# Optimization experiments

Hardware: AMD Instinct MI355X
Metric: run time of the kernel (lower is better)

## Reference

```python
import jax, jax.numpy as jnp
import numpy as np

B, H = 8, 8
C_IN, C_OUT = 128, 128
E, O = C_IN // H, C_OUT // H              # per-head channels
S = (32, 32, 64)                           # spatial dims (space_dims_q == space_dims_kv)
M = (8, 8, 8)                              # lowest-mode block kept per rfft dim
N_MODES = M[0] * M[1] * M[2]               # 512 = mask.sum()
SCALE = 1.0 / (C_IN * C_OUT)


def setup_inputs() -> dict:
    key = jax.random.key(0)
    k1, k2, k3, k4 = jax.random.split(key, 4)
    q = jax.random.normal(k1, (B, H, E) + S, dtype=jnp.float32)
    k = jax.random.normal(k2, (B, H, E) + S, dtype=jnp.float32)
    # torch.rand(..., dtype=cfloat): real and imag parts each uniform [0,1), scaled
    w_re = jax.random.uniform(k3, (H, E, O, N_MODES), dtype=jnp.float32) * SCALE
    w_im = jax.random.uniform(k4, (H, E, O, N_MODES), dtype=jnp.float32) * SCALE
    return {"q": q, "k": k, "w_re": w_re, "w_im": w_im}


def _select_modes(x_ft):
    # block low-mode mask -> slice + flatten (C order, matches torch bool indexing)
    m0, m1, m2 = M
    return x_ft[..., :m0, :m1, :m2].reshape(x_ft.shape[:3] + (-1,))


def reference(q, k, w_re, w_im):
    m0, m1, m2 = M
    xq_ft = jnp.fft.rfftn(q, axes=(3, 4, 5), norm='ortho')   # [B,H,E,32,32,33] c64
    xk_ft = jnp.fft.rfftn(k, axes=(3, 4, 5), norm='ortho')
    xq_sel = _select_modes(xq_ft)                             # [B,H,E,Mq]
    xk_sel = _select_modes(xk_ft)                             # [B,H,E,Mkv]
    w = jax.lax.complex(w_re, w_im)                           # [H,E,O,Mq]

    # complex attention: no conjugation, complex tanh (matches torch)
    att = jnp.tanh(jnp.einsum('bhex,bhey->bhxy', xq_sel, xk_sel))
    xqkv = jnp.einsum('bhxy,bhey->bhex', att, xk_sel)         # [B,H,E,Mq]
    xqkvw = jnp.einsum('bhex,heox->bhox', xqkv, w)            # [B,H,O,Mq]

    out_ft = jnp.zeros((q.shape[0], H, O, S[0], S[1], S[2] // 2 + 1),
                       dtype=xqkvw.dtype)
    out_ft = out_ft.at[..., :m0, :m1, :m2].set(
        xqkvw.reshape(q.shape[0], H, O, m0, m1, m2))

    # canonical_fft_freq over dims (3,4): x <- (x + conj(x[-i mod s0, -j mod s1]))/2
    neg = jnp.roll(jnp.flip(out_ft, axis=(3, 4)), shift=(1, 1), axis=(3, 4))
    out_ft = (out_ft + jnp.conj(neg)) * 0.5

    out = jnp.fft.irfftn(out_ft / (C_IN * C_OUT), axes=(3, 4, 5), s=S, norm='ortho')
    return out  # original returns (out, None)
```

## Files before the change

kernel.cpp:

```cpp
#include <hip/hip_runtime.h>

#define PI_F 3.14159265358979323846f

template<int v> struct ic_t { static constexpr int value = v; };

template<int N, int I = 0, typename F>
__device__ __forceinline__ void sfor(F&& f) {
  if constexpr (I < N) { f(ic_t<I>{}); sfor<N, I + 1>(static_cast<F&&>(f)); }
}

__host__ __device__ constexpr int fold_idx(int t) {
  t &= 63;
  return (t <= 16) ? t : (t <= 32) ? (32 - t) : (t <= 48) ? (t - 32) : (64 - t);
}
__host__ __device__ constexpr float fold_sgn(int t) {
  t &= 63;
  return (t <= 16) ? 1.f : (t <= 48) ? -1.f : 1.f;
}

__device__ constexpr float CCV[17] = {
  1.0f, 0.9951847266721969f, 0.9807852804032304f, 0.9569403357322088f,
  0.9238795325112867f, 0.8819212643483550f, 0.8314696123025452f,
  0.7730104533627370f, 0.7071067811865476f, 0.6343932841636455f,
  0.5555702330196022f, 0.4713967368259976f, 0.3826834323650898f,
  0.2902846772544623f, 0.1950903220161283f, 0.0980171403295606f, 0.0f};

#define TCOS(T) (fold_sgn(T) * CCV[fold_idx(T)])
#define TSIN(T) (fold_sgn(((T) + 48) & 63) * CCV[fold_idx(((T) + 48) & 63)])

__global__ __launch_bounds__(512)
void k1_fwd_dft(const float* __restrict__ qg, const float* __restrict__ kg,
                float2* __restrict__ qsel, float2* __restrict__ ksel)
{
  __shared__ float2 A[8192];
  __shared__ float2 tw64[64];

  const int tid = threadIdx.x;
  const int lane = tid & 63;
  const int wv = tid >> 6;
  const int bid = blockIdx.x;
  const int t1023 = bid & 1023;
  const float* __restrict__ src = (bid < 1024 ? qg : kg) + (size_t)t1023 * 65536;
  float2* __restrict__ dst = (bid < 1024 ? qsel : ksel) + t1023 * 512;

  if (tid < 64) {
    float s, c;
    sincosf((float)tid * (2.f * PI_F / 64.f), &s, &c);
    tw64[tid] = make_float2(c, s);
  }

  const int n1b = wv * 2 + (lane >> 5);
  const int n2h = lane & 31;
  const float2* __restrict__ sp = (const float2*)src + n1b * 32 + n2h;

  float Br[8], Bi[8];
  sfor<8>([&](auto K) { constexpr int k = decltype(K)::value;
    Br[k] = 0.f; Bi[k] = 0.f; });

  sfor<2>([&](auto CH) {
    constexpr int chunk = decltype(CH)::value;
    float aR[2][8], aI[2][8];
    sfor<8>([&](auto K) { constexpr int k = decltype(K)::value;
      aR[0][k] = 0.f; aI[0][k] = 0.f; aR[1][k] = 0.f; aI[1][k] = 0.f; });
    const float2* __restrict__ spc = sp + chunk * 512;
    sfor<16>([&](auto NP) {
      constexpr int n0p = decltype(NP)::value;
      const float2 a = spc[n0p * 1024];
      const float2 b = spc[(n0p + 16) * 1024];
      const float sx = a.x + b.x, sy = a.y + b.y;
      const float dx = a.x - b.x, dy = a.y - b.y;
      sfor<8>([&](auto KC) {
        constexpr int k0 = decltype(KC)::value;
        constexpr int t = (2 * k0 * n0p) & 63;
        const float gx = (k0 & 1) ? dx : sx;
        const float gy = (k0 & 1) ? dy : sy;
        aR[0][k0] = fmaf(gx,  TCOS(t), aR[0][k0]);
        aI[0][k0] = fmaf(-gx, TSIN(t), aI[0][k0]);
        aR[1][k0] = fmaf(gy,  TCOS(t), aR[1][k0]);
        aI[1][k0] = fmaf(-gy, TSIN(t), aI[1][k0]);
      });
    });
    sfor<8>([&](auto KC) {
      constexpr int k0 = decltype(KC)::value;
      float4* p = (float4*)&A[(n1b * 8 + k0) * 64 + 2 * n2h];
      *p = make_float4(aR[0][k0], aI[0][k0], aR[1][k0], aI[1][k0]);
    });
    __syncthreads();
    sfor<16>([&](auto NL) {
      constexpr int n1l = decltype(NL)::value;
      const int tt = (2 * wv * (chunk * 16 + n1l)) & 63;
      const float2 w = tw64[tt];
      sfor<8>([&](auto KC) {
        constexpr int k0 = decltype(KC)::value;
        const float2 a = A[(n1l * 8 + k0) * 64 + lane];
        Br[k0] = fmaf(a.x, w.x, fmaf( a.y, w.y, Br[k0]));
        Bi[k0] = fmaf(a.y, w.x, fmaf(-a.x, w.y, Bi[k0]));
      });
    });
    __syncthreads();
  });

  sfor<8>([&](auto KC) {
    constexpr int k0 = decltype(KC)::value;
    A[(wv * 8 + k0) * 65 + lane] = make_float2(Br[k0], Bi[k0]);
  });
  __syncthreads();

  {
    const float2* __restrict__ rb = &A[lane * 65];
    float oR = 0.f, oI = 0.f;
    #pragma unroll 8
    for (int n2 = 0; n2 < 64; ++n2) {
      const float2 b = rb[n2];
      const float2 w = tw64[(wv * n2) & 63];
      oR = fmaf(b.x, w.x, fmaf( b.y, w.y, oR));
      oI = fmaf(b.y, w.x, fmaf(-b.x, w.y, oI));
    }
    dst[((lane & 7) << 6) + ((lane >> 3) << 3) + wv] =
        make_float2(oR * (1.f / 256.f), oI * (1.f / 256.f));
  }
}

__global__ __launch_bounds__(512, 4)
void k2_attn(const float2* __restrict__ qsel, const float2* __restrict__ ksel,
             float2* __restrict__ xqkv)
{
  __shared__ float2 Kl[8192];
  const int tid = threadIdx.x;
  const int bh = blockIdx.x >> 3;
  const int xo = blockIdx.x & 7;

  const float2* __restrict__ kb = ksel + bh * 8192;
  for (int i = tid; i < 8192; i += 512) Kl[i] = kb[i];

  const int xr = tid & 63;
  const int yh = tid >> 6;
  const int x = xo * 64 + xr;
  const float2* __restrict__ qb = qsel + bh * 8192;
  float qr[16], qi[16], ar[16], ai[16];
  sfor<16>([&](auto E) {
    constexpr int e = decltype(E)::value;
    const float2 v = qb[e * 512 + x];
    qr[e] = v.x; qi[e] = v.y;
    ar[e] = 0.f; ai[e] = 0.f;
  });
  __syncthreads();

  const int y0 = yh * 64;
  for (int y = y0; y < y0 + 64; ++y) {
    float kr[16], ki[16];
    float sr = 0.f, si = 0.f;
    sfor<16>([&](auto E) {
      constexpr int e = decltype(E)::value;
      const float2 v = Kl[e * 512 + y];
      kr[e] = v.x; ki[e] = v.y;
      sr = fmaf(qr[e], v.x, fmaf(-qi[e], v.y, sr));
      si = fmaf(qr[e], v.y, fmaf( qi[e], v.x, si));
    });
    float a2 = 2.f * sr;
    a2 = fminf(fmaxf(a2, -30.f), 30.f);
    const float b2 = 2.f * si;
    const float ea = expf(a2);
    const float ei = 1.f / ea;
    const float sh = 0.5f * (ea - ei);
    const float chp = 0.5f * (ea + ei);
    float sb, cb;
    sincosf(b2, &sb, &cb);
    const float inv = 1.f / (chp + cb);
    const float tr = sh * inv;
    const float ti = sb * inv;
    sfor<16>([&](auto E) {
      constexpr int e = decltype(E)::value;
      ar[e] = fmaf(tr, kr[e], fmaf(-ti, ki[e], ar[e]));
      ai[e] = fmaf(tr, ki[e], fmaf( ti, kr[e], ai[e]));
    });
  }
  __syncthreads();
  float* __restrict__ red = (float*)Kl;
  if (yh) {
    const int g = yh - 1;
    sfor<16>([&](auto E) {
      constexpr int e = decltype(E)::value;
      red[(g * 32 + 2 * e) * 64 + xr] = ar[e];
      red[(g * 32 + 2 * e + 1) * 64 + xr] = ai[e];
    });
  }
  __syncthreads();
  if (!yh) {
    float2* __restrict__ ob = xqkv + bh * 8192;
    sfor<16>([&](auto E) {
      constexpr int e = decltype(E)::value;
      float sr2 = ar[e], si2 = ai[e];
      #pragma unroll
      for (int g = 0; g < 7; ++g) {
        sr2 += red[(g * 32 + 2 * e) * 64 + xr];
        si2 += red[(g * 32 + 2 * e + 1) * 64 + xr];
      }
      ob[e * 512 + x] = make_float2(sr2, si2);
    });
  }
}

#define SCALE_OUT (1.f / 4194304.f)

__global__ __launch_bounds__(256, 2)
void k3_inv(const float2* __restrict__ xqkv, const float* __restrict__ w_re,
            const float* __restrict__ w_im, float* __restrict__ out)
{
  __shared__ float2 Fs[512];
  __shared__ float cn[64];
  __shared__ float Ur[4096], Ui[4096];
  __shared__ float Vr[2048], Vi[2048];

  const int tid = threadIdx.x;
  const int bho = blockIdx.x;
  const int o = bho & 15;
  const int h = (bho >> 4) & 7;
  const int bh = bho >> 4;

  if (tid < 64) cn[tid] = cosf((float)tid * (PI_F / 32.f));

  float cc[17];
  sfor<17>([&](auto J) { constexpr int j = decltype(J)::value;
    cc[j] = cosf((float)j * (PI_F / 32.f)); });
  #define TCOSr(T) (fold_sgn(T) * cc[fold_idx(T)])
  #define TSINr(T) (fold_sgn(((T) + 48) & 63) * cc[fold_idx(((T) + 48) & 63)])

  const float2* __restrict__ xb = xqkv + bh * 8192;
  const float* __restrict__ wrb = w_re + ((size_t)(h * 256 + o)) * 512;
  const float* __restrict__ wib = w_im + ((size_t)(h * 256 + o)) * 512;
  for (int x = tid; x < 512; x += 256) {
    float fr = 0.f, fi = 0.f;
    sfor<16>([&](auto E) {
      constexpr int e = decltype(E)::value;
      const float2 v = xb[e * 512 + x];
      const float wr = wrb[e * 8192 + x];
      const float wi = wib[e * 8192 + x];
      fr = fmaf(v.x, wr, fmaf(-v.y, wi, fr));
      fi = fmaf(v.x, wi, fmaf( v.y, wr, fi));
    });
    Fs[x] = make_float2(fr * SCALE_OUT, fi * SCALE_OUT);
  }
  __syncthreads();

  const int n2 = tid & 63;
  const int wv = tid >> 6;

  #pragma unroll
  for (int i = 0; i < 16; ++i) {
    const int p = wv * 16 + i;
    float ur = 0.f, ui = 0.f;
    sfor<8>([&](auto KC) {
      constexpr int k2 = decltype(KC)::value;
      const float2 f = Fs[p * 8 + k2];
      const float cv = cn[(k2 * n2) & 63];
      const float wgt = (k2 == 0) ? cv : 2.f * cv;
      ur = fmaf(wgt, f.x, ur);
      ui = fmaf(wgt, f.y, ui);
    });
    Ur[p * 64 + n2] = ur;
    Ui[p * 64 + n2] = ui;
  }
  __syncthreads();

  float u_r[2][8], u_i[2][8];
  sfor<2>([&](auto JC) {
    constexpr int j = decltype(JC)::value;
    sfor<8>([&](auto KC) {
      constexpr int k1 = decltype(KC)::value;
      const int p = (wv * 2 + j) * 8 + k1;
      u_r[j][k1] = Ur[p * 64 + n2];
      u_i[j][k1] = Ui[p * 64 + n2];
    });
  });

  float* __restrict__ ob = out + (size_t)bho * 65536;

  for (int chq = 0; chq < 8; ++chq) {
    sfor<2>([&](auto JC) {
      constexpr int j = decltype(JC)::value;
      const int k0 = wv * 2 + j;
      sfor<4>([&](auto LC) {
        constexpr int l = decltype(LC)::value;
        const int n1 = chq * 4 + l;
        float vr = 0.f, vi = 0.f;
        sfor<8>([&](auto KC) {
          constexpr int k1 = decltype(KC)::value;
          const int t = (2 * k1 * n1) & 63;
          const float cv = cn[t];
          const float sv = cn[(t + 48) & 63];
          vr = fmaf(u_r[j][k1], cv, fmaf(-u_i[j][k1], sv, vr));
          vi = fmaf(u_r[j][k1], sv, fmaf( u_i[j][k1], cv, vi));
        });
        Vr[(k0 * 4 + l) * 64 + n2] = vr;
        Vi[(k0 * 4 + l) * 64 + n2] = vi;
      });
    });
    __syncthreads();
    {
      const int l = wv;
      float vrr[8], vii[8];
      sfor<8>([&](auto KC) {
        constexpr int k0 = decltype(KC)::value;
        vrr[k0] = Vr[(k0 * 4 + l) * 64 + n2];
        vii[k0] = Vi[(k0 * 4 + l) * 64 + n2];
      });
      const int n1 = chq * 4 + l;
      float* __restrict__ op = ob + n1 * 64 + n2;
      sfor<32>([&](auto NC) {
        constexpr int n0 = decltype(NC)::value;
        float acc = vrr[0];
        sfor<7>([&](auto KC) {
          constexpr int k0 = decltype(KC)::value + 1;
          constexpr int t = (2 * k0 * n0) & 63;
          acc = fmaf(vrr[k0], TCOSr(t), fmaf(-vii[k0], TSINr(t), acc));
        });
        op[n0 * 2048] = acc;
      });
    }
    __syncthreads();
  }
}

extern "C" void kernel_launch(void* const* d_in, const int* in_sizes, int n_in,
                              void* d_out, int out_size, void* d_ws, size_t ws_size,
                              hipStream_t stream)
{
  (void)in_sizes; (void)n_in; (void)out_size; (void)ws_size;
  const float* q    = (const float*)d_in[0];
  const float* k    = (const float*)d_in[1];
  const float* w_re = (const float*)d_in[2];
  const float* w_im = (const float*)d_in[3];
  float* out = (float*)d_out;

  float2* qsel = (float2*)d_ws;
  float2* ksel = qsel + 1024 * 512;
  float2* xqkv = ksel + 1024 * 512;

  hipLaunchKernelGGL(k1_fwd_dft, dim3(2048), dim3(512), 0, stream, q, k, qsel, ksel);
  hipLaunchKernelGGL(k2_attn,    dim3(512),  dim3(512), 0, stream, qsel, ksel, xqkv);
  hipLaunchKernelGGL(k3_inv,     dim3(1024), dim3(256), 0, stream, xqkv, w_re, w_im, out);
}
```

Measured before the change: 327.2 us.

## Halve forward-DFT shared memory with smaller chunks and swizzled transpose buffer

Restructures the first forward DFT stage so each wave handles one n1 row per chunk with scalar float loads, processed in four chunks of 8 rows instead of two chunks of 16 paired rows. The shared buffer drops from 8192 to 4096 float2, and the padded (65-stride) transpose is replaced by an XOR-free rotation swizzle so it fits in the smaller buffer. The aim is lower LDS and register use per block, allowing more resident blocks, at the cost of extra barriers and narrower global loads.

```diff
diff --git a/kernel.cpp b/kernel.cpp
--- a/kernel.cpp
+++ b/kernel.cpp
@@ -32,7 +32,7 @@
 void k1_fwd_dft(const float* __restrict__ qg, const float* __restrict__ kg,
                 float2* __restrict__ qsel, float2* __restrict__ ksel)
 {
-  __shared__ float2 A[8192];
+  __shared__ float2 A[4096];
   __shared__ float2 tw64[64];
 
   const int tid = threadIdx.x;
@@ -49,46 +49,41 @@
     tw64[tid] = make_float2(c, s);
   }
 
-  const int n1b = wv * 2 + (lane >> 5);
-  const int n2h = lane & 31;
-  const float2* __restrict__ sp = (const float2*)src + n1b * 32 + n2h;
-
   float Br[8], Bi[8];
   sfor<8>([&](auto K) { constexpr int k = decltype(K)::value;
     Br[k] = 0.f; Bi[k] = 0.f; });
 
-  sfor<2>([&](auto CH) {
+  sfor<4>([&](auto CH) {
     constexpr int chunk = decltype(CH)::value;
-    float aR[2][8], aI[2][8];
-    sfor<8>([&](auto K) { constexpr int k = decltype(K)::value;
-      aR[0][k] = 0.f; aI[0][k] = 0.f; aR[1][k] = 0.f; aI[1][k] = 0.f; });
-    const float2* __restrict__ spc = sp + chunk * 512;
-    sfor<16>([&](auto NP) {
-      constexpr int n0p = decltype(NP)::value;
-      const float2 a = spc[n0p * 1024];
-      const float2 b = spc[(n0p + 16) * 1024];
-      const float sx = a.x + b.x, sy = a.y + b.y;
-      const float dx = a.x - b.x, dy = a.y - b.y;
+    {
+      const int n1 = chunk * 8 + wv;
+      const float* __restrict__ rp = src + n1 * 64 + lane;
+      float aR[8], aI[8];
+      sfor<8>([&](auto K) { constexpr int k = decltype(K)::value;
+        aR[k] = 0.f; aI[k] = 0.f; });
+      sfor<16>([&](auto NP) {
+        constexpr int n0p = decltype(NP)::value;
+        const float a = rp[n0p * 2048];
+        const float b = rp[(n0p + 16) * 2048];
+        const float s = a + b;
+        const float d = a - b;
+        sfor<8>([&](auto KC) {
+          constexpr int k0 = decltype(KC)::value;
+          constexpr int t = (2 * k0 * n0p) & 63;
+          const float g = (k0 & 1) ? d : s;
+          aR[k0] = fmaf(g,  TCOS(t), aR[k0]);
+          aI[k0] = fmaf(-g, TSIN(t), aI[k0]);
+        });
+      });
       sfor<8>([&](auto KC) {
         constexpr int k0 = decltype(KC)::value;
-        constexpr int t = (2 * k0 * n0p) & 63;
-        const float gx = (k0 & 1) ? dx : sx;
-        const float gy = (k0 & 1) ? dy : sy;
-        aR[0][k0] = fmaf(gx,  TCOS(t), aR[0][k0]);
-        aI[0][k0] = fmaf(-gx, TSIN(t), aI[0][k0]);
-        aR[1][k0] = fmaf(gy,  TCOS(t), aR[1][k0]);
-        aI[1][k0] = fmaf(-gy, TSIN(t), aI[1][k0]);
-      });
-    });
-    sfor<8>([&](auto KC) {
-      constexpr int k0 = decltype(KC)::value;
-      float4* p = (float4*)&A[(n1b * 8 + k0) * 64 + 2 * n2h];
-      *p = make_float4(aR[0][k0], aI[0][k0], aR[1][k0], aI[1][k0]);
-    });
+        A[(wv * 8 + k0) * 64 + lane] = make_float2(aR[k0], aI[k0]);
+      });
+    }
     __syncthreads();
-    sfor<16>([&](auto NL) {
+    sfor<8>([&](auto NL) {
       constexpr int n1l = decltype(NL)::value;
-      const int tt = (2 * wv * (chunk * 16 + n1l)) & 63;
+      const int tt = (2 * wv * (chunk * 8 + n1l)) & 63;
       const float2 w = tw64[tt];
       sfor<8>([&](auto KC) {
         constexpr int k0 = decltype(KC)::value;
@@ -102,16 +97,16 @@
 
   sfor<8>([&](auto KC) {
     constexpr int k0 = decltype(KC)::value;
-    A[(wv * 8 + k0) * 65 + lane] = make_float2(Br[k0], Bi[k0]);
+    const int row = wv * 8 + k0;
+    A[row * 64 + ((lane + row) & 63)] = make_float2(Br[k0], Bi[k0]);
   });
   __syncthreads();
 
   {
-    const float2* __restrict__ rb = &A[lane * 65];
     float oR = 0.f, oI = 0.f;
     #pragma unroll 8
     for (int n2 = 0; n2 < 64; ++n2) {
-      const float2 b = rb[n2];
+      const float2 b = A[lane * 64 + ((n2 + lane) & 63)];
       const float2 w = tw64[(wv * n2) & 63];
       oR = fmaf(b.x, w.x, fmaf( b.y, w.y, oR));
       oI = fmaf(b.y, w.x, fmaf(-b.x, w.y, oI));
```

After: 329.3 us. Within noise of the previous version (+0.6%).
